# Kernel optimization log

Hardware: AMD Instinct MI355X
Metric: run time of the kernel (lower is better)

The kernel has to match this reference:

```python
import jax, jax.numpy as jnp
import numpy as np

N_NODES = 50000
N_EDGES = 800000
NUM_FEATURES = 128
HIDDEN = 128
EMBED = 64
OUT_DIM = 1


def setup_inputs() -> dict:
    key = jax.random.key(0)
    ks = jax.random.split(key, 12)
    x = jax.random.normal(ks[0], (N_NODES, NUM_FEATURES), dtype=jnp.float32)
    edge_index = jax.random.randint(ks[1], (2, N_EDGES), 0, N_NODES, dtype=jnp.int64)

    def glorot(k, fan_in, fan_out):
        s = jnp.sqrt(6.0 / (fan_in + fan_out)).astype(jnp.float32)
        return jax.random.uniform(k, (fan_in, fan_out), jnp.float32, -s, s)

    return {
        "x": x,
        "edge_index": edge_index,
        "W1": glorot(ks[2], NUM_FEATURES, HIDDEN),
        "b1": jnp.zeros((HIDDEN,), jnp.float32),
        "Wh": glorot(ks[3], HIDDEN, HIDDEN),
        "bh": jnp.zeros((HIDDEN,), jnp.float32),
        "W2": glorot(ks[4], HIDDEN, EMBED),
        "b2": jnp.zeros((EMBED,), jnp.float32),
        "Wout": glorot(ks[5], EMBED, OUT_DIM),
        "bout": jnp.zeros((OUT_DIM,), jnp.float32),
    }


def _gcn_norm(edge_index, num_nodes):
    # Add self-loops, compute symmetric normalization deg^{-1/2} A_hat deg^{-1/2}
    loop = jnp.arange(num_nodes, dtype=edge_index.dtype)
    src = jnp.concatenate([edge_index[0], loop])
    dst = jnp.concatenate([edge_index[1], loop])
    deg = jax.ops.segment_sum(jnp.ones_like(dst, dtype=jnp.float32), dst,
                              num_segments=num_nodes)
    dis = jnp.where(deg > 0, jax.lax.rsqrt(jnp.maximum(deg, 1.0)), 0.0)
    norm = dis[src] * dis[dst]  # [E+N]
    return src, dst, norm


def _gcn_conv(h, W, b, src, dst, norm, num_nodes):
    h = h @ W  # linear transform first (PyG GCNConv)
    msg = h[src] * norm[:, None]  # gather + scale
    return jax.ops.segment_sum(msg, dst, num_segments=num_nodes) + b


def reference(x, edge_index, W1, b1, Wh, bh, W2, b2, Wout, bout):
    n = x.shape[0]
    src, dst, norm = _gcn_norm(edge_index, n)
    h = jax.nn.relu(_gcn_conv(x, W1, b1, src, dst, norm, n))  # dropout p=0 -> identity
    h = jax.nn.relu(_gcn_conv(h, Wh, bh, src, dst, norm, n))
    h = _gcn_conv(h, W2, b2, src, dst, norm, n)
    out = h @ Wout + bout
    return (out, h)
```

## Files before the change

kernel.cpp:

```cpp
#include <hip/hip_runtime.h>
#include <hip/hip_bf16.h>


#define N_NODES 50000
#define N_EDGES 800000
#define NBUCK 196
#define GB 196
#define EPB 4096

typedef __attribute__((ext_vector_type(8))) short short8;
typedef __attribute__((ext_vector_type(4))) float f32x4;

static __device__ __forceinline__ unsigned short f2bf(float f) {
    __hip_bfloat16 h = __float2bfloat16(f);
    return *reinterpret_cast<unsigned short*>(&h);
}
static __device__ __forceinline__ float bf2f(unsigned short u) {
    return __uint_as_float(((unsigned)u) << 16);
}


__global__ __launch_bounds__(256) void hist_wprep_kernel(
    const int* __restrict__ dstv, int* __restrict__ H, int nE, int* __restrict__ ticket,
    const float* __restrict__ W1, const float* __restrict__ Wh, const float* __restrict__ W2,
    unsigned short* __restrict__ W1hi, unsigned short* __restrict__ W1lo,
    unsigned short* __restrict__ Whhi, unsigned short* __restrict__ Whlo,
    unsigned short* __restrict__ W2hi, unsigned short* __restrict__ W2lo) {
    int gt = blockIdx.x * 256 + threadIdx.x;
    if (gt == 0) *ticket = 0;
    if (gt < 40960) {
        const float* W;
        unsigned short *Hi, *Lo;
        int nout, lt;
        if (gt < 16384)      { W = W1; Hi = W1hi; Lo = W1lo; nout = 128; lt = gt; }
        else if (gt < 32768) { W = Wh; Hi = Whhi; Lo = Whlo; nout = 128; lt = gt - 16384; }
        else                 { W = W2; Hi = W2hi; Lo = W2lo; nout = 64;  lt = gt - 32768; }
        int col = lt % nout, k = lt / nout;
        float v = W[lt];
        unsigned short hi = f2bf(v);
        unsigned short lo = f2bf(v - bf2f(hi));
        Hi[(size_t)col * 128 + k] = hi;
        Lo[(size_t)col * 128 + k] = lo;
    }

    __shared__ int h[NBUCK];
    for (int i = threadIdx.x; i < NBUCK; i += 256) h[i] = 0;
    __syncthreads();
    int base = blockIdx.x * EPB;
#pragma unroll
    for (int i = 0; i < EPB / 256; ++i) {
        int e = base + i * 256 + threadIdx.x;
        if (e < nE) atomicAdd(&h[dstv[e] >> 8], 1);
    }
    __syncthreads();
    for (int i = threadIdx.x; i < NBUCK; i += 256)
        H[i * GB + blockIdx.x] = h[i];
}

__global__ __launch_bounds__(256) void scan_kernel(int* __restrict__ H,
                                                   int* __restrict__ bsum,
                                                   int* __restrict__ bstart,
                                                   int* __restrict__ rowoff_last,
                                                   int* __restrict__ ticket) {
    __shared__ int s[256];
    __shared__ int lastFlag;
    int t = threadIdx.x;
    int k = blockIdx.x;
    int v = (t < GB) ? H[k * GB + t] : 0;
    s[t] = v;
    __syncthreads();
    for (int off = 1; off < 256; off <<= 1) {
        int u = (t >= off) ? s[t - off] : 0;
        __syncthreads();
        s[t] += u;
        __syncthreads();
    }
    if (t < GB) H[k * GB + t] = s[t] - v;
    if (t == 255) {
        bsum[k] = s[255];
        __threadfence();
        int tk = atomicAdd(ticket, 1);
        lastFlag = (tk == NBUCK - 1);
    }
    __syncthreads();
    if (!lastFlag) return;
    __threadfence();
    int v2 = (t < NBUCK) ? bsum[t] : 0;
    s[t] = v2;
    __syncthreads();
    for (int off = 1; off < 256; off <<= 1) {
        int u = (t >= off) ? s[t - off] : 0;
        __syncthreads();
        s[t] += u;
        __syncthreads();
    }
    if (t < NBUCK) bstart[t] = s[t] - v2;
    if (t == 0) {
        bstart[NBUCK] = N_EDGES;
        *rowoff_last = N_EDGES;
    }
}

__global__ __launch_bounds__(256) void partition_kernel(const int* __restrict__ srcv,
                                                        const int* __restrict__ dstv,
                                                        const int* __restrict__ H,
                                                        const int* __restrict__ bstart,
                                                        unsigned int* __restrict__ P, int nE) {
    __shared__ int cur[NBUCK];
    for (int i = threadIdx.x; i < NBUCK; i += 256)
        cur[i] = bstart[i] + H[i * GB + blockIdx.x];
    __syncthreads();
    int base = blockIdx.x * EPB;
#pragma unroll
    for (int i = 0; i < EPB / 256; ++i) {
        int e = base + i * 256 + threadIdx.x;
        if (e < nE) {
            int d = dstv[e];
            unsigned int pk = (unsigned int)srcv[e] | ((unsigned int)(d & 255) << 16);
            int pos = atomicAdd(&cur[d >> 8], 1);
            P[pos] = pk;
        }
    }
}

__global__ __launch_bounds__(256) void bucket_csr_kernel(const unsigned int* __restrict__ P,
                                                         const int* __restrict__ bstart,
                                                         int* __restrict__ rowoff,
                                                         float* __restrict__ dis,
                                                         int* __restrict__ csr_src, int n) {
    __shared__ int cnt[256];
    __shared__ int s[256];
    __shared__ int cur[256];
    int t = threadIdx.x;
    int k = blockIdx.x;
    int ebeg = bstart[k], eend = bstart[k + 1];
    cnt[t] = 0;
    __syncthreads();
    for (int e = ebeg + t; e < eend; e += 256)
        atomicAdd(&cnt[(P[e] >> 16) & 255], 1);
    __syncthreads();
    int myc = cnt[t];
    s[t] = myc;
    __syncthreads();
    for (int off = 1; off < 256; off <<= 1) {
        int v = (t >= off) ? s[t - off] : 0;
        __syncthreads();
        s[t] += v;
        __syncthreads();
    }
    int excl = s[t] - myc;
    int node = (k << 8) + t;
    if (node < n) {
        rowoff[node] = ebeg + excl;
        dis[node] = rsqrtf((float)(myc + 1));
    }
    cur[t] = ebeg + excl;
    __syncthreads();
    for (int e = ebeg + t; e < eend; e += 256) {
        unsigned int p = P[e];
        int pos = atomicAdd(&cur[(p >> 16) & 255], 1);
        csr_src[pos] = (int)(p & 0xFFFFu);
    }
}

template <int NOUT>
__global__ __launch_bounds__(256) void gemm_mfma_kernel(
    const float* __restrict__ A,
    const unsigned short* __restrict__ Wthi,
    const unsigned short* __restrict__ Wtlo,
    const float* __restrict__ scale,
    unsigned short* __restrict__ C, int M) {
    constexpr int LDK = 136;
    __shared__ unsigned short sAhi[64 * LDK];
    __shared__ unsigned short sAlo[64 * LDK];

    int tid = threadIdx.x;
    int w = tid >> 6, lane = tid & 63;
    int quad = lane >> 4, m = lane & 15;
    int Rbase = blockIdx.x * 64;
    int r0 = (w & 1) * 32, c0 = (w >> 1) * 32;

    short8 bh[4][2], bl[4][2];
    f32x4 acc00, acc01, acc10, acc11;

    auto loadB = [&](int CB) {
#pragma unroll
        for (int ks = 0; ks < 4; ++ks)
#pragma unroll
            for (int g = 0; g < 2; ++g) {
                size_t off = (size_t)(CB + c0 + g * 16 + m) * 128 + ks * 32 + quad * 8;
                bh[ks][g] = *(const short8*)(Wthi + off);
                bl[ks][g] = *(const short8*)(Wtlo + off);
            }
    };

    auto kloop = [&]() {
#pragma unroll
        for (int ks = 0; ks < 4; ++ks) {
            int kof = ks * 32 + quad * 8;
            short8 ah0 = *(const short8*)(sAhi + (r0 + m) * LDK + kof);
            short8 ah1 = *(const short8*)(sAhi + (r0 + 16 + m) * LDK + kof);
            short8 al0 = *(const short8*)(sAlo + (r0 + m) * LDK + kof);
            short8 al1 = *(const short8*)(sAlo + (r0 + 16 + m) * LDK + kof);
            acc00 = __builtin_amdgcn_mfma_f32_16x16x32_bf16(ah0, bh[ks][0], acc00, 0, 0, 0);
            acc01 = __builtin_amdgcn_mfma_f32_16x16x32_bf16(ah0, bh[ks][1], acc01, 0, 0, 0);
            acc10 = __builtin_amdgcn_mfma_f32_16x16x32_bf16(ah1, bh[ks][0], acc10, 0, 0, 0);
            acc11 = __builtin_amdgcn_mfma_f32_16x16x32_bf16(ah1, bh[ks][1], acc11, 0, 0, 0);
            acc00 = __builtin_amdgcn_mfma_f32_16x16x32_bf16(ah0, bl[ks][0], acc00, 0, 0, 0);
            acc01 = __builtin_amdgcn_mfma_f32_16x16x32_bf16(ah0, bl[ks][1], acc01, 0, 0, 0);
            acc10 = __builtin_amdgcn_mfma_f32_16x16x32_bf16(ah1, bl[ks][0], acc10, 0, 0, 0);
            acc11 = __builtin_amdgcn_mfma_f32_16x16x32_bf16(ah1, bl[ks][1], acc11, 0, 0, 0);
            acc00 = __builtin_amdgcn_mfma_f32_16x16x32_bf16(al0, bh[ks][0], acc00, 0, 0, 0);
            acc01 = __builtin_amdgcn_mfma_f32_16x16x32_bf16(al0, bh[ks][1], acc01, 0, 0, 0);
            acc10 = __builtin_amdgcn_mfma_f32_16x16x32_bf16(al1, bh[ks][0], acc10, 0, 0, 0);
            acc11 = __builtin_amdgcn_mfma_f32_16x16x32_bf16(al1, bh[ks][1], acc11, 0, 0, 0);
        }
    };

    auto writeC = [&](int CB) {
#pragma unroll
        for (int reg = 0; reg < 4; ++reg) {
            int row0g = Rbase + r0 + quad * 4 + reg;
            if (row0g < M) {
                float sc = scale[row0g];
                C[(size_t)row0g * NOUT + CB + c0 + m]      = f2bf(acc00[reg] * sc);
                C[(size_t)row0g * NOUT + CB + c0 + 16 + m] = f2bf(acc01[reg] * sc);
            }
            int row1g = row0g + 16;
            if (row1g < M) {
                float sc = scale[row1g];
                C[(size_t)row1g * NOUT + CB + c0 + m]      = f2bf(acc10[reg] * sc);
                C[(size_t)row1g * NOUT + CB + c0 + 16 + m] = f2bf(acc11[reg] * sc);
            }
        }
    };

    loadB(0);

    for (int i = tid; i < 64 * 32; i += 256) {
        int r = i >> 5, c4 = i & 31;
        int row = Rbase + r;
        float4 v = make_float4(0.f, 0.f, 0.f, 0.f);
        if (row < M) v = ((const float4*)(A + (size_t)row * 128))[c4];
        ushort4 hi, lo;
        hi.x = f2bf(v.x); lo.x = f2bf(v.x - bf2f(hi.x));
        hi.y = f2bf(v.y); lo.y = f2bf(v.y - bf2f(hi.y));
        hi.z = f2bf(v.z); lo.z = f2bf(v.z - bf2f(hi.z));
        hi.w = f2bf(v.w); lo.w = f2bf(v.w - bf2f(hi.w));
        *(ushort4*)(sAhi + r * LDK + c4 * 4) = hi;
        *(ushort4*)(sAlo + r * LDK + c4 * 4) = lo;
    }
    __syncthreads();

    f32x4 z = {0.f, 0.f, 0.f, 0.f};
    acc00 = z; acc01 = z; acc10 = z; acc11 = z;
    kloop();
    if constexpr (NOUT == 128) loadB(64);
    writeC(0);
    if constexpr (NOUT == 128) {
        acc00 = z; acc01 = z; acc10 = z; acc11 = z;
        kloop();
        writeC(64);
    }
}

__global__ __launch_bounds__(256) void aggregate128_kernel(
    const int* __restrict__ rowoff, const int* __restrict__ csr_src,
    const float* __restrict__ dis, const unsigned short* __restrict__ tp,
    const float* __restrict__ bias, float* __restrict__ hout, int n) {
    int wid = (blockIdx.x * 256 + threadIdx.x) >> 6;
    int lane = threadIdx.x & 63;
    int h = lane >> 5, lc = lane & 31;
    int n0 = wid * 2;
    if (n0 >= n) return;
    int n1 = n0 + 1;
    bool has1 = (n1 < n);

    float a0[4] = {0.f, 0.f, 0.f, 0.f};
    float a1[4] = {0.f, 0.f, 0.f, 0.f};

#define ROW128(node) (*((const ushort4*)(tp + (size_t)(node) * 128) + lc))
#define ACC(a, u) { a[0] += bf2f(u.x); a[1] += bf2f(u.y); a[2] += bf2f(u.z); a[3] += bf2f(u.w); }

    if (h == 0) { ushort4 u = ROW128(n0); ACC(a0, u); }
    else if (has1) { ushort4 u = ROW128(n1); ACC(a1, u); }

    int mid = rowoff[n0 + 1];
    int i0 = rowoff[n0] + h;
    int i1 = mid + h;
    int end1 = has1 ? rowoff[n1 + 1] : mid;

    while (i0 + 6 < mid && i1 + 6 < end1) {
        int p0 = csr_src[i0], p1 = csr_src[i0 + 2], p2 = csr_src[i0 + 4], p3 = csr_src[i0 + 6];
        int q0 = csr_src[i1], q1 = csr_src[i1 + 2], q2 = csr_src[i1 + 4], q3 = csr_src[i1 + 6];
        ushort4 u0 = ROW128(p0), u1 = ROW128(p1), u2 = ROW128(p2), u3 = ROW128(p3);
        ushort4 v0 = ROW128(q0), v1 = ROW128(q1), v2 = ROW128(q2), v3 = ROW128(q3);
        ACC(a0, u0); ACC(a0, u1); ACC(a0, u2); ACC(a0, u3);
        ACC(a1, v0); ACC(a1, v1); ACC(a1, v2); ACC(a1, v3);
        i0 += 8; i1 += 8;
    }
    while (i0 + 2 < mid && i1 + 2 < end1) {
        int p0 = csr_src[i0], p1 = csr_src[i0 + 2];
        int q0 = csr_src[i1], q1 = csr_src[i1 + 2];
        ushort4 u0 = ROW128(p0), u1 = ROW128(p1);
        ushort4 v0 = ROW128(q0), v1 = ROW128(q1);
        ACC(a0, u0); ACC(a0, u1);
        ACC(a1, v0); ACC(a1, v1);
        i0 += 4; i1 += 4;
    }
    for (; i0 + 2 < mid; i0 += 4) {
        int p0 = csr_src[i0], p1 = csr_src[i0 + 2];
        ushort4 u0 = ROW128(p0), u1 = ROW128(p1);
        ACC(a0, u0); ACC(a0, u1);
    }
    for (; i0 < mid; i0 += 2) { ushort4 u = ROW128(csr_src[i0]); ACC(a0, u); }
    for (; i1 + 2 < end1; i1 += 4) {
        int q0 = csr_src[i1], q1 = csr_src[i1 + 2];
        ushort4 v0 = ROW128(q0), v1 = ROW128(q1);
        ACC(a1, v0); ACC(a1, v1);
    }
    for (; i1 < end1; i1 += 2) { ushort4 v = ROW128(csr_src[i1]); ACC(a1, v); }
#undef ROW128
#undef ACC

#pragma unroll
    for (int j = 0; j < 4; ++j) {
        a0[j] += __shfl_xor(a0[j], 32);
        a1[j] += __shfl_xor(a1[j], 32);
    }

    float4 b = ((const float4*)bias)[lc];
    if (h == 0) {
        float dd = dis[n0];
        float4 r;
        r.x = fmaxf(a0[0] * dd + b.x, 0.f);
        r.y = fmaxf(a0[1] * dd + b.y, 0.f);
        r.z = fmaxf(a0[2] * dd + b.z, 0.f);
        r.w = fmaxf(a0[3] * dd + b.w, 0.f);
        ((float4*)(hout + (size_t)n0 * 128))[lc] = r;
    } else if (has1) {
        float dd = dis[n1];
        float4 r;
        r.x = fmaxf(a1[0] * dd + b.x, 0.f);
        r.y = fmaxf(a1[1] * dd + b.y, 0.f);
        r.z = fmaxf(a1[2] * dd + b.z, 0.f);
        r.w = fmaxf(a1[3] * dd + b.w, 0.f);
        ((float4*)(hout + (size_t)n1 * 128))[lc] = r;
    }
}

__global__ __launch_bounds__(256) void aggregate64_head_kernel(
    const int* __restrict__ rowoff, const int* __restrict__ csr_src,
    const float* __restrict__ dis, const unsigned short* __restrict__ tp,
    const float* __restrict__ bias, const float* __restrict__ Wout,
    const float* __restrict__ bout, float* __restrict__ hout,
    float* __restrict__ out, int n) {
    int wid = (blockIdx.x * 256 + threadIdx.x) >> 6;
    int lane = threadIdx.x & 63;
    int h = lane >> 5, lc = lane & 31;
    int n0 = wid * 2;
    if (n0 >= n) return;
    int n1 = n0 + 1;
    bool has1 = (n1 < n);

    float a0[2] = {0.f, 0.f};
    float a1[2] = {0.f, 0.f};

#define ROW64(node) (*((const ushort2*)(tp + (size_t)(node) * 64) + lc))
#define ACC2(a, u) { a[0] += bf2f(u.x); a[1] += bf2f(u.y); }

    if (h == 0) { ushort2 u = ROW64(n0); ACC2(a0, u); }
    else if (has1) { ushort2 u = ROW64(n1); ACC2(a1, u); }

    int mid = rowoff[n0 + 1];
    int i0 = rowoff[n0] + h;
    int i1 = mid + h;
    int end1 = has1 ? rowoff[n1 + 1] : mid;

    while (i0 + 6 < mid && i1 + 6 < end1) {
        int p0 = csr_src[i0], p1 = csr_src[i0 + 2], p2 = csr_src[i0 + 4], p3 = csr_src[i0 + 6];
        int q0 = csr_src[i1], q1 = csr_src[i1 + 2], q2 = csr_src[i1 + 4], q3 = csr_src[i1 + 6];
        ushort2 u0 = ROW64(p0), u1 = ROW64(p1), u2 = ROW64(p2), u3 = ROW64(p3);
        ushort2 v0 = ROW64(q0), v1 = ROW64(q1), v2 = ROW64(q2), v3 = ROW64(q3);
        ACC2(a0, u0); ACC2(a0, u1); ACC2(a0, u2); ACC2(a0, u3);
        ACC2(a1, v0); ACC2(a1, v1); ACC2(a1, v2); ACC2(a1, v3);
        i0 += 8; i1 += 8;
    }
    while (i0 + 2 < mid && i1 + 2 < end1) {
        int p0 = csr_src[i0], p1 = csr_src[i0 + 2];
        int q0 = csr_src[i1], q1 = csr_src[i1 + 2];
        ushort2 u0 = ROW64(p0), u1 = ROW64(p1);
        ushort2 v0 = ROW64(q0), v1 = ROW64(q1);
        ACC2(a0, u0); ACC2(a0, u1);
        ACC2(a1, v0); ACC2(a1, v1);
        i0 += 4; i1 += 4;
    }
    for (; i0 < mid; i0 += 2) { ushort2 u = ROW64(csr_src[i0]); ACC2(a0, u); }
    for (; i1 < end1; i1 += 2) { ushort2 v = ROW64(csr_src[i1]); ACC2(a1, v); }
#undef ROW64
#undef ACC2

#pragma unroll
    for (int j = 0; j < 2; ++j) {
        a0[j] += __shfl_xor(a0[j], 32);
        a1[j] += __shfl_xor(a1[j], 32);
    }

    int node = h ? n1 : n0;
    float* ap = h ? a1 : a0;
    bool valid = (h == 0) || has1;
    float2 hv = make_float2(0.f, 0.f);
    if (valid) {
        float dd = dis[node];
        float2 b = ((const float2*)bias)[lc];
        hv.x = ap[0] * dd + b.x;
        hv.y = ap[1] * dd + b.y;
        ((float2*)(hout + (size_t)node * 64))[lc] = hv;
    }
    float2 wv = ((const float2*)Wout)[lc];
    float p = valid ? (hv.x * wv.x + hv.y * wv.y) : 0.f;
#pragma unroll
    for (int off = 16; off > 0; off >>= 1) p += __shfl_down(p, off);
    if (lc == 0 && valid) out[node] = p + bout[0];
}

extern "C" void kernel_launch(void* const* d_in, const int* in_sizes, int n_in,
                              void* d_out, int out_size, void* d_ws, size_t ws_size,
                              hipStream_t stream) {
    const float* x    = (const float*)d_in[0];
    const int*   ei   = (const int*)d_in[1];
    const float* W1   = (const float*)d_in[2];
    const float* b1   = (const float*)d_in[3];
    const float* Wh   = (const float*)d_in[4];
    const float* bh   = (const float*)d_in[5];
    const float* W2   = (const float*)d_in[6];
    const float* b2   = (const float*)d_in[7];
    const float* Wout = (const float*)d_in[8];
    const float* bout = (const float*)d_in[9];

    const int N = N_NODES;
    const int E = N_EDGES;
    const int* srcv = ei;
    const int* dstv = ei + E;

    float* out  = (float*)d_out;
    float* hout = (float*)d_out + N;

    char* ws = (char*)d_ws;
    int*   H       = (int*)ws;                          ws += sizeof(int) * NBUCK * GB;
    int*   bsum    = (int*)ws;                          ws += sizeof(int) * NBUCK;
    int*   bstart  = (int*)ws;                          ws += sizeof(int) * (NBUCK + 1);
    int*   ticket  = (int*)ws;                          ws += sizeof(int) * 4;
    int*   rowoff  = (int*)ws;                          ws += sizeof(int) * (N + 1);
    unsigned int* P = (unsigned int*)ws;                ws += sizeof(unsigned int) * E;
    int*   csr_src = (int*)ws;                          ws += sizeof(int) * E;
    float* dis     = (float*)ws;                        ws += sizeof(float) * N;
    unsigned short* W1thi = (unsigned short*)ws;        ws += sizeof(unsigned short) * 128 * 128;
    unsigned short* W1tlo = (unsigned short*)ws;        ws += sizeof(unsigned short) * 128 * 128;
    unsigned short* Whthi = (unsigned short*)ws;        ws += sizeof(unsigned short) * 128 * 128;
    unsigned short* Whtlo = (unsigned short*)ws;        ws += sizeof(unsigned short) * 128 * 128;
    unsigned short* W2thi = (unsigned short*)ws;        ws += sizeof(unsigned short) * 64 * 128;
    unsigned short* W2tlo = (unsigned short*)ws;        ws += sizeof(unsigned short) * 64 * 128;
    unsigned short* bufT  = (unsigned short*)ws;        ws += sizeof(unsigned short) * (size_t)N * 128;
    float* bufH    = (float*)ws;

    hist_wprep_kernel<<<GB, 256, 0, stream>>>(dstv, H, E, ticket,
                                              W1, Wh, W2, W1thi, W1tlo, Whthi, Whtlo, W2thi, W2tlo);
    scan_kernel<<<NBUCK, 256, 0, stream>>>(H, bsum, bstart, rowoff + N, ticket);
    partition_kernel<<<GB, 256, 0, stream>>>(srcv, dstv, H, bstart, P, E);
    bucket_csr_kernel<<<NBUCK, 256, 0, stream>>>(P, bstart, rowoff, dis, csr_src, N);

    const int aggBlocks = ((N + 1) / 2 * 64 + 255) / 256;
    const int gemmRows = (N + 63) / 64;

    gemm_mfma_kernel<128><<<gemmRows, 256, 0, stream>>>(x, W1thi, W1tlo, dis, bufT, N);
    aggregate128_kernel<<<aggBlocks, 256, 0, stream>>>(rowoff, csr_src, dis, bufT, b1, bufH, N);

    gemm_mfma_kernel<128><<<gemmRows, 256, 0, stream>>>(bufH, Whthi, Whtlo, dis, bufT, N);
    aggregate128_kernel<<<aggBlocks, 256, 0, stream>>>(rowoff, csr_src, dis, bufT, bh, bufH, N);

    gemm_mfma_kernel<64><<<gemmRows, 256, 0, stream>>>(bufH, W2thi, W2tlo, dis, bufT, N);
    aggregate64_head_kernel<<<aggBlocks, 256, 0, stream>>>(
        rowoff, csr_src, dis, bufT, b2, Wout, bout, hout, out, N);
}
```

Measured before the change: 304.0 us.

## Store hidden activations as bf16 hi/lo split, 16-bit CSR indices, 2D GEMM grid

The aggregation kernel now writes its activations already split into bf16 hi and lo halves, so the next GEMM loads them directly instead of reading fp32 and converting. CSR source indices are stored as 16-bit values, which halves index traffic in the gather. The GEMM also splits its output columns across a second grid dimension for more blocks. The cost is that the A tile is loaded twice when columns are split, and the 16-bit index relies on packing that already holds only 16 bits of the source id while N is 50000.

```diff
diff --git a/kernel.cpp b/kernel.cpp
--- a/kernel.cpp
+++ b/kernel.cpp
@@ -127,7 +127,7 @@
                                                          const int* __restrict__ bstart,
                                                          int* __restrict__ rowoff,
                                                          float* __restrict__ dis,
-                                                         int* __restrict__ csr_src, int n) {
+                                                         unsigned short* __restrict__ csr_src, int n) {
     __shared__ int cnt[256];
     __shared__ int s[256];
     __shared__ int cur[256];
@@ -159,13 +159,15 @@
     for (int e = ebeg + t; e < eend; e += 256) {
         unsigned int p = P[e];
         int pos = atomicAdd(&cur[(p >> 16) & 255], 1);
-        csr_src[pos] = (int)(p & 0xFFFFu);
-    }
-}
-
-template <int NOUT>
+        csr_src[pos] = (unsigned short)(p & 0xFFFFu);
+    }
+}
+
+template <int NOUT, bool SPLITA>
 __global__ __launch_bounds__(256) void gemm_mfma_kernel(
     const float* __restrict__ A,
+    const unsigned short* __restrict__ Ahi,
+    const unsigned short* __restrict__ Alo,
     const unsigned short* __restrict__ Wthi,
     const unsigned short* __restrict__ Wtlo,
     const float* __restrict__ scale,
@@ -178,96 +180,95 @@
     int w = tid >> 6, lane = tid & 63;
     int quad = lane >> 4, m = lane & 15;
     int Rbase = blockIdx.x * 64;
+    int Cbase = blockIdx.y * 64;
     int r0 = (w & 1) * 32, c0 = (w >> 1) * 32;
 
     short8 bh[4][2], bl[4][2];
-    f32x4 acc00, acc01, acc10, acc11;
-
-    auto loadB = [&](int CB) {
-#pragma unroll
-        for (int ks = 0; ks < 4; ++ks)
-#pragma unroll
-            for (int g = 0; g < 2; ++g) {
-                size_t off = (size_t)(CB + c0 + g * 16 + m) * 128 + ks * 32 + quad * 8;
-                bh[ks][g] = *(const short8*)(Wthi + off);
-                bl[ks][g] = *(const short8*)(Wtlo + off);
+#pragma unroll
+    for (int ks = 0; ks < 4; ++ks)
+#pragma unroll
+        for (int g = 0; g < 2; ++g) {
+            size_t off = (size_t)(Cbase + c0 + g * 16 + m) * 128 + ks * 32 + quad * 8;
+            bh[ks][g] = *(const short8*)(Wthi + off);
+            bl[ks][g] = *(const short8*)(Wtlo + off);
+        }
+
+    if constexpr (SPLITA) {
+        for (int i = tid; i < 64 * 16; i += 256) {
+            int r = i >> 4, c8 = i & 15;
+            int row = Rbase + r;
+            short8 hv = {0, 0, 0, 0, 0, 0, 0, 0};
+            short8 lv = {0, 0, 0, 0, 0, 0, 0, 0};
+            if (row < M) {
+                hv = *(const short8*)(Ahi + (size_t)row * 128 + c8 * 8);
+                lv = *(const short8*)(Alo + (size_t)row * 128 + c8 * 8);
             }
-    };
-
-    auto kloop = [&]() {
-#pragma unroll
-        for (int ks = 0; ks < 4; ++ks) {
-            int kof = ks * 32 + quad * 8;
-            short8 ah0 = *(const short8*)(sAhi + (r0 + m) * LDK + kof);
-            short8 ah1 = *(const short8*)(sAhi + (r0 + 16 + m) * LDK + kof);
-            short8 al0 = *(const short8*)(sAlo + (r0 + m) * LDK + kof);
-            short8 al1 = *(const short8*)(sAlo + (r0 + 16 + m) * LDK + kof);
-            acc00 = __builtin_amdgcn_mfma_f32_16x16x32_bf16(ah0, bh[ks][0], acc00, 0, 0, 0);
-            acc01 = __builtin_amdgcn_mfma_f32_16x16x32_bf16(ah0, bh[ks][1], acc01, 0, 0, 0);
-            acc10 = __builtin_amdgcn_mfma_f32_16x16x32_bf16(ah1, bh[ks][0], acc10, 0, 0, 0);
-            acc11 = __builtin_amdgcn_mfma_f32_16x16x32_bf16(ah1, bh[ks][1], acc11, 0, 0, 0);
-            acc00 = __builtin_amdgcn_mfma_f32_16x16x32_bf16(ah0, bl[ks][0], acc00, 0, 0, 0);
-            acc01 = __builtin_amdgcn_mfma_f32_16x16x32_bf16(ah0, bl[ks][1], acc01, 0, 0, 0);
-            acc10 = __builtin_amdgcn_mfma_f32_16x16x32_bf16(ah1, bl[ks][0], acc10, 0, 0, 0);
-            acc11 = __builtin_amdgcn_mfma_f32_16x16x32_bf16(ah1, bl[ks][1], acc11, 0, 0, 0);
-            acc00 = __builtin_amdgcn_mfma_f32_16x16x32_bf16(al0, bh[ks][0], acc00, 0, 0, 0);
-            acc01 = __builtin_amdgcn_mfma_f32_16x16x32_bf16(al0, bh[ks][1], acc01, 0, 0, 0);
-            acc10 = __builtin_amdgcn_mfma_f32_16x16x32_bf16(al1, bh[ks][0], acc10, 0, 0, 0);
-            acc11 = __builtin_amdgcn_mfma_f32_16x16x32_bf16(al1, bh[ks][1], acc11, 0, 0, 0);
-        }
-    };
-
-    auto writeC = [&](int CB) {
-#pragma unroll
-        for (int reg = 0; reg < 4; ++reg) {
-            int row0g = Rbase + r0 + quad * 4 + reg;
-            if (row0g < M) {
-                float sc = scale[row0g];
-                C[(size_t)row0g * NOUT + CB + c0 + m]      = f2bf(acc00[reg] * sc);
-                C[(size_t)row0g * NOUT + CB + c0 + 16 + m] = f2bf(acc01[reg] * sc);
-            }
-            int row1g = row0g + 16;
-            if (row1g < M) {
-                float sc = scale[row1g];
-                C[(size_t)row1g * NOUT + CB + c0 + m]      = f2bf(acc10[reg] * sc);
-                C[(size_t)row1g * NOUT + CB + c0 + 16 + m] = f2bf(acc11[reg] * sc);
-            }
-        }
-    };
-
-    loadB(0);
-
-    for (int i = tid; i < 64 * 32; i += 256) {
-        int r = i >> 5, c4 = i & 31;
-        int row = Rbase + r;
-        float4 v = make_float4(0.f, 0.f, 0.f, 0.f);
-        if (row < M) v = ((const float4*)(A + (size_t)row * 128))[c4];
-        ushort4 hi, lo;
-        hi.x = f2bf(v.x); lo.x = f2bf(v.x - bf2f(hi.x));
-        hi.y = f2bf(v.y); lo.y = f2bf(v.y - bf2f(hi.y));
-        hi.z = f2bf(v.z); lo.z = f2bf(v.z - bf2f(hi.z));
-        hi.w = f2bf(v.w); lo.w = f2bf(v.w - bf2f(hi.w));
-        *(ushort4*)(sAhi + r * LDK + c4 * 4) = hi;
-        *(ushort4*)(sAlo + r * LDK + c4 * 4) = lo;
+            *(short8*)(sAhi + r * LDK + c8 * 8) = hv;
+            *(short8*)(sAlo + r * LDK + c8 * 8) = lv;
+        }
+    } else {
+        for (int i = tid; i < 64 * 32; i += 256) {
+            int r = i >> 5, c4 = i & 31;
+            int row = Rbase + r;
+            float4 v = make_float4(0.f, 0.f, 0.f, 0.f);
+            if (row < M) v = ((const float4*)(A + (size_t)row * 128))[c4];
+            ushort4 hi, lo;
+            hi.x = f2bf(v.x); lo.x = f2bf(v.x - bf2f(hi.x));
+            hi.y = f2bf(v.y); lo.y = f2bf(v.y - bf2f(hi.y));
+            hi.z = f2bf(v.z); lo.z = f2bf(v.z - bf2f(hi.z));
+            hi.w = f2bf(v.w); lo.w = f2bf(v.w - bf2f(hi.w));
+            *(ushort4*)(sAhi + r * LDK + c4 * 4) = hi;
+            *(ushort4*)(sAlo + r * LDK + c4 * 4) = lo;
+        }
     }
     __syncthreads();
 
     f32x4 z = {0.f, 0.f, 0.f, 0.f};
-    acc00 = z; acc01 = z; acc10 = z; acc11 = z;
-    kloop();
-    if constexpr (NOUT == 128) loadB(64);
-    writeC(0);
-    if constexpr (NOUT == 128) {
-        acc00 = z; acc01 = z; acc10 = z; acc11 = z;
-        kloop();
-        writeC(64);
+    f32x4 acc00 = z, acc01 = z, acc10 = z, acc11 = z;
+
+#pragma unroll
+    for (int ks = 0; ks < 4; ++ks) {
+        int kof = ks * 32 + quad * 8;
+        short8 ah0 = *(const short8*)(sAhi + (r0 + m) * LDK + kof);
+        short8 ah1 = *(const short8*)(sAhi + (r0 + 16 + m) * LDK + kof);
+        short8 al0 = *(const short8*)(sAlo + (r0 + m) * LDK + kof);
+        short8 al1 = *(const short8*)(sAlo + (r0 + 16 + m) * LDK + kof);
+        acc00 = __builtin_amdgcn_mfma_f32_16x16x32_bf16(ah0, bh[ks][0], acc00, 0, 0, 0);
+        acc01 = __builtin_amdgcn_mfma_f32_16x16x32_bf16(ah0, bh[ks][1], acc01, 0, 0, 0);
+        acc10 = __builtin_amdgcn_mfma_f32_16x16x32_bf16(ah1, bh[ks][0], acc10, 0, 0, 0);
+        acc11 = __builtin_amdgcn_mfma_f32_16x16x32_bf16(ah1, bh[ks][1], acc11, 0, 0, 0);
+        acc00 = __builtin_amdgcn_mfma_f32_16x16x32_bf16(ah0, bl[ks][0], acc00, 0, 0, 0);
+        acc01 = __builtin_amdgcn_mfma_f32_16x16x32_bf16(ah0, bl[ks][1], acc01, 0, 0, 0);
+        acc10 = __builtin_amdgcn_mfma_f32_16x16x32_bf16(ah1, bl[ks][0], acc10, 0, 0, 0);
+        acc11 = __builtin_amdgcn_mfma_f32_16x16x32_bf16(ah1, bl[ks][1], acc11, 0, 0, 0);
+        acc00 = __builtin_amdgcn_mfma_f32_16x16x32_bf16(al0, bh[ks][0], acc00, 0, 0, 0);
+        acc01 = __builtin_amdgcn_mfma_f32_16x16x32_bf16(al0, bh[ks][1], acc01, 0, 0, 0);
+        acc10 = __builtin_amdgcn_mfma_f32_16x16x32_bf16(al1, bh[ks][0], acc10, 0, 0, 0);
+        acc11 = __builtin_amdgcn_mfma_f32_16x16x32_bf16(al1, bh[ks][1], acc11, 0, 0, 0);
+    }
+
+#pragma unroll
+    for (int reg = 0; reg < 4; ++reg) {
+        int row0g = Rbase + r0 + quad * 4 + reg;
+        if (row0g < M) {
+            float sc = scale[row0g];
+            C[(size_t)row0g * NOUT + Cbase + c0 + m]      = f2bf(acc00[reg] * sc);
+            C[(size_t)row0g * NOUT + Cbase + c0 + 16 + m] = f2bf(acc01[reg] * sc);
+        }
+        int row1g = row0g + 16;
+        if (row1g < M) {
+            float sc = scale[row1g];
+            C[(size_t)row1g * NOUT + Cbase + c0 + m]      = f2bf(acc10[reg] * sc);
+            C[(size_t)row1g * NOUT + Cbase + c0 + 16 + m] = f2bf(acc11[reg] * sc);
+        }
     }
 }
 
 __global__ __launch_bounds__(256) void aggregate128_kernel(
-    const int* __restrict__ rowoff, const int* __restrict__ csr_src,
+    const int* __restrict__ rowoff, const unsigned short* __restrict__ csr_src,
     const float* __restrict__ dis, const unsigned short* __restrict__ tp,
-    const float* __restrict__ bias, float* __restrict__ hout, int n) {
+    const float* __restrict__ bias,
+    unsigned short* __restrict__ outHi, unsigned short* __restrict__ outLo, int n) {
     int wid = (blockIdx.x * 256 + threadIdx.x) >> 6;
     int lane = threadIdx.x & 63;
     int h = lane >> 5, lc = lane & 31;
@@ -330,27 +331,28 @@
     }
 
     float4 b = ((const float4*)bias)[lc];
-    if (h == 0) {
-        float dd = dis[n0];
+    float* ap = (h == 0) ? a0 : a1;
+    int node = (h == 0) ? n0 : n1;
+    bool valid = (h == 0) || has1;
+    if (valid) {
+        float dd = dis[node];
         float4 r;
-        r.x = fmaxf(a0[0] * dd + b.x, 0.f);
-        r.y = fmaxf(a0[1] * dd + b.y, 0.f);
-        r.z = fmaxf(a0[2] * dd + b.z, 0.f);
-        r.w = fmaxf(a0[3] * dd + b.w, 0.f);
-        ((float4*)(hout + (size_t)n0 * 128))[lc] = r;
-    } else if (has1) {
-        float dd = dis[n1];
-        float4 r;
-        r.x = fmaxf(a1[0] * dd + b.x, 0.f);
-        r.y = fmaxf(a1[1] * dd + b.y, 0.f);
-        r.z = fmaxf(a1[2] * dd + b.z, 0.f);
-        r.w = fmaxf(a1[3] * dd + b.w, 0.f);
-        ((float4*)(hout + (size_t)n1 * 128))[lc] = r;
+        r.x = fmaxf(ap[0] * dd + b.x, 0.f);
+        r.y = fmaxf(ap[1] * dd + b.y, 0.f);
+        r.z = fmaxf(ap[2] * dd + b.z, 0.f);
+        r.w = fmaxf(ap[3] * dd + b.w, 0.f);
+        ushort4 hi, lo;
+        hi.x = f2bf(r.x); lo.x = f2bf(r.x - bf2f(hi.x));
+        hi.y = f2bf(r.y); lo.y = f2bf(r.y - bf2f(hi.y));
+        hi.z = f2bf(r.z); lo.z = f2bf(r.z - bf2f(hi.z));
+        hi.w = f2bf(r.w); lo.w = f2bf(r.w - bf2f(hi.w));
+        ((ushort4*)(outHi + (size_t)node * 128))[lc] = hi;
+        ((ushort4*)(outLo + (size_t)node * 128))[lc] = lo;
     }
 }
 
 __global__ __launch_bounds__(256) void aggregate64_head_kernel(
-    const int* __restrict__ rowoff, const int* __restrict__ csr_src,
+    const int* __restrict__ rowoff, const unsigned short* __restrict__ csr_src,
     const float* __restrict__ dis, const unsigned short* __restrict__ tp,
     const float* __restrict__ bias, const float* __restrict__ Wout,
     const float* __restrict__ bout, float* __restrict__ hout,
@@ -453,7 +455,7 @@
     int*   ticket  = (int*)ws;                          ws += sizeof(int) * 4;
     int*   rowoff  = (int*)ws;                          ws += sizeof(int) * (N + 1);
     unsigned int* P = (unsigned int*)ws;                ws += sizeof(unsigned int) * E;
-    int*   csr_src = (int*)ws;                          ws += sizeof(int) * E;
+    unsigned short* csr_src = (unsigned short*)ws;      ws += sizeof(unsigned short) * (E + 2);
     float* dis     = (float*)ws;                        ws += sizeof(float) * N;
     unsigned short* W1thi = (unsigned short*)ws;        ws += sizeof(unsigned short) * 128 * 128;
     unsigned short* W1tlo = (unsigned short*)ws;        ws += sizeof(unsigned short) * 128 * 128;
@@ -462,7 +464,8 @@
     unsigned short* W2thi = (unsigned short*)ws;        ws += sizeof(unsigned short) * 64 * 128;
     unsigned short* W2tlo = (unsigned short*)ws;        ws += sizeof(unsigned short) * 64 * 128;
     unsigned short* bufT  = (unsigned short*)ws;        ws += sizeof(unsigned short) * (size_t)N * 128;
-    float* bufH    = (float*)ws;
+    unsigned short* bufHi = (unsigned short*)ws;        ws += sizeof(unsigned short) * (size_t)N * 128;
+    unsigned short* bufLo = (unsigned short*)ws;
 
     hist_wprep_kernel<<<GB, 256, 0, stream>>>(dstv, H, E, ticket,
                                               W1, Wh, W2, W1thi, W1tlo, Whthi, Whtlo, W2thi, W2tlo);
@@ -473,13 +476,18 @@
     const int aggBlocks = ((N + 1) / 2 * 64 + 255) / 256;
     const int gemmRows = (N + 63) / 64;
 
-    gemm_mfma_kernel<128><<<gemmRows, 256, 0, stream>>>(x, W1thi, W1tlo, dis, bufT, N);
-    aggregate128_kernel<<<aggBlocks, 256, 0, stream>>>(rowoff, csr_src, dis, bufT, b1, bufH, N);
-
-    gemm_mfma_kernel<128><<<gemmRows, 256, 0, stream>>>(bufH, Whthi, Whtlo, dis, bufT, N);
-    aggregate128_kernel<<<aggBlocks, 256, 0, stream>>>(rowoff, csr_src, dis, bufT, bh, bufH, N);
-
-    gemm_mfma_kernel<64><<<gemmRows, 256, 0, stream>>>(bufH, W2thi, W2tlo, dis, bufT, N);
+    gemm_mfma_kernel<128, false><<<dim3(gemmRows, 2), 256, 0, stream>>>(
+        x, nullptr, nullptr, W1thi, W1tlo, dis, bufT, N);
+    aggregate128_kernel<<<aggBlocks, 256, 0, stream>>>(
+        rowoff, csr_src, dis, bufT, b1, bufHi, bufLo, N);
+
+    gemm_mfma_kernel<128, true><<<dim3(gemmRows, 2), 256, 0, stream>>>(
+        nullptr, bufHi, bufLo, Whthi, Whtlo, dis, bufT, N);
+    aggregate128_kernel<<<aggBlocks, 256, 0, stream>>>(
+        rowoff, csr_src, dis, bufT, bh, bufHi, bufLo, N);
+
+    gemm_mfma_kernel<64, true><<<dim3(gemmRows, 1), 256, 0, stream>>>(
+        nullptr, bufHi, bufLo, W2thi, W2tlo, dis, bufT, N);
     aggregate64_head_kernel<<<aggBlocks, 256, 0, stream>>>(
         rowoff, csr_src, dis, bufT, b2, Wout, bout, hout, out, N);
 }
```

New measurement: 290.3 us. 1.05x faster.
